# Optimization experiments

Hardware: AMD Instinct MI355X
Metric: run time of the kernel (lower is better)

Reference implementation:

```python
import jax, jax.numpy as jnp
import numpy as np

B, NUMS, SEQ, H, LAYERS, PRED = 128, 128, 256, 1024, 2, 96


def setup_inputs() -> dict:
    key = jax.random.key(0)
    ks = jax.random.split(key, 7)
    s = 0.02
    return {
        "x": jax.random.normal(ks[0], (B, NUMS, SEQ), jnp.float32),
        "W0": jax.random.normal(ks[1], (NUMS + H, 4 * H), jnp.float32) * s,
        "b0": jax.random.normal(ks[2], (4 * H,), jnp.float32) * s,
        "W1": jax.random.normal(ks[3], (H + H, 4 * H), jnp.float32) * s,
        "b1": jax.random.normal(ks[4], (4 * H,), jnp.float32) * s,
        "fc_w": jax.random.normal(ks[5], (H, PRED), jnp.float32) * s,
        "fc_b": jax.random.normal(ks[6], (PRED,), jnp.float32) * s,
    }


def _lstm_layer(x_seq, W, b, h0, c0):
    # x_seq: [B, T, D]; W packs the four gate linears [D+H, 4H] (i,f,o,g)
    def step(carry, xt):
        h, c = carry
        z = jnp.concatenate([xt, h], axis=1) @ W + b  # [B, 4H]
        i, f, o, g = jnp.split(z, 4, axis=1)
        i, f, o = jax.nn.sigmoid(i), jax.nn.sigmoid(f), jax.nn.sigmoid(o)
        c = f * c + i * jnp.tanh(g)
        h = o * jnp.tanh(c)
        return (h, c), h

    (h, c), hs = jax.lax.scan(step, (h0, c0), jnp.swapaxes(x_seq, 0, 1))
    return jnp.swapaxes(hs, 0, 1), h, c  # [B, T, H], [B, H], [B, H]


def reference(x, W0, b0, W1, b1, fc_w, fc_b):
    bsz = x.shape[0]
    h = jnp.zeros((bsz, H), x.dtype)
    c = jnp.zeros((bsz, H), x.dtype)
    seq = jnp.swapaxes(x, 1, 2)  # [B, T, NUMS]
    # NB: faithful to source, (h, c) carry over across layers (no reset)
    seq, h, c = _lstm_layer(seq, W0, b0, h, c)
    seq, h, c = _lstm_layer(seq, W1, b1, h, c)
    out = jnp.tanh(seq[:, -1, :] @ fc_w + fc_b)  # [B, PRED]
    return (out, h, c)
```

## Files before the change

### kernel.cpp

```cpp
#include <hip/hip_runtime.h>
#include <stdint.h>

#define Bsz  128
#define NUMS 128
#define SEQn 256
#define Hn   1024
#define PRED 96
#define G4H  4096
#define GN   256
#define BH   ((size_t)Bsz*Hn)

typedef __attribute__((ext_vector_type(8))) short bf16x8;
typedef __attribute__((ext_vector_type(4))) float f32x4;

template<int N> struct IC { static constexpr int value = N; };

__device__ __forceinline__ unsigned short f2bf(float x){
  union { float f; unsigned u; } v; v.f = x;
  return (unsigned short)((v.u + 0x7FFFu + ((v.u >> 16) & 1u)) >> 16);
}

__global__ void pack_x_kernel(const float* __restrict__ x, unsigned short* __restrict__ xp){
  __shared__ float tile[64][65];
  const int t0 = blockIdx.x * 64, n0 = blockIdx.y * 64, b = blockIdx.z;
  const int tid = threadIdx.x;
  const int c = tid & 63, r = tid >> 6;
  #pragma unroll
  for (int i = 0; i < 16; i++){
    int n = r + i*4;
    tile[n][c] = x[((size_t)b*NUMS + n0 + n)*SEQn + t0 + c];
  }
  __syncthreads();
  #pragma unroll
  for (int i = 0; i < 16; i++){
    int t = r + i*4;
    xp[((size_t)(t0+t)*Bsz + b)*NUMS + n0 + c] = f2bf(tile[c][t]);
  }
}

__global__ void pack_w_kernel(const float* __restrict__ W, unsigned short* __restrict__ Wpk,
                              int KST, int row_off, int kstride, int kof){
  const int u = blockIdx.x * blockDim.x + threadIdx.x;
  if (u >= 256*KST*64) return;
  const int lane = u & 63;
  const int kst  = (u >> 6) % KST;
  const int cgg  = (u >> 6) / KST;
  const int nb = cgg >> 2, gate = cgg & 3;
  const int col = gate*Hn + nb*16 + (lane & 15);
  const int kbase = row_off + kst*32 + (lane >> 4)*8;
  unsigned short tmp[8];
  #pragma unroll
  for (int e = 0; e < 8; e++) tmp[e] = f2bf(W[(size_t)(kbase+e)*G4H + col]);
  ((ulonglong2*)Wpk)[(size_t)(cgg*kstride + kof + kst)*64 + lane] = *(const ulonglong2*)tmp;
}

__global__ void zero_kernel(unsigned short* __restrict__ h0, float* __restrict__ c,
                            unsigned* __restrict__ bars){
  int i = blockIdx.x*256 + threadIdx.x;
  if (i < Bsz*Hn){ h0[i] = 0; c[i] = 0.0f; }
  if (i < 2048) bars[i] = 0u;
}

template<int K1, int S2, int KTOT, int LAYER, bool RING2>
__global__ __launch_bounds__(512, 2)
void persist_kernel(const unsigned short* __restrict__ xpp,
                    unsigned short* __restrict__ hring,
                    unsigned short* __restrict__ h1b,
                    const unsigned short* __restrict__ Wpk,
                    const float* __restrict__ bias,
                    float* __restrict__ cst,
                    float* __restrict__ hf_out,
                    unsigned* __restrict__ bar)
{
  constexpr int KST_TOT = KTOT/32;
  constexpr int HALF = KST_TOT/2;
  constexpr int NCH = (KTOT + 511)/512;
  constexpr int NBUF = (LAYER == 0) ? 2 : 4;
  __shared__ unsigned short sa[NBUF][32*512];
  __shared__ unsigned short sxb[(LAYER == 0) ? 32*128 : 64];
  __shared__ float se[2][4*32*18];

  const int tid = threadIdx.x;
  const int w = tid >> 6, l = tid & 63;
  const int blk = blockIdx.x;
  const int q = blk >> 3;
  const int nb = (blk & 7)*8 + (q & 7);
  const int mb = q >> 3;
  const int ksh = w & 1, cgi = w >> 1;
  const int cgg = nb*4 + cgi;
  const int lrow = l & 15, lg = l >> 4;
  const int bgrp = blk >> 3;

  bf16x8 wreg[HALF];
  #pragma unroll
  for (int j = 0; j < HALF; j++)
    wreg[j] = *(const bf16x8*)(Wpk + ((size_t)(cgg*KST_TOT + 2*j + ksh)*64 + l)*8);

  const int erow = tid >> 4, ejj = tid & 15;
  const int R = mb*32 + erow;
  const int J = nb*16 + ejj;
  const size_t idx = (size_t)R*Hn + J;
  float creg = (LAYER == 0) ? 0.f : cst[idx];

  for (int t = 0; t < SEQn; ++t){
    #pragma unroll
    for (int j = 0; j < HALF; j++) asm volatile("" : "+v"(wreg[j]));

    const unsigned short* A1;
    const unsigned short* A2;
    unsigned short* hout;
    if (LAYER == 0){
      A1   = hring + (size_t)t*BH;
      A2   = xpp + (size_t)t*Bsz*NUMS;
      hout = hring + (size_t)(t+1)*BH;
    } else {
      A1   = hring + (size_t)(t+1)*BH;
      A2   = (t == 0) ? (hring + (size_t)SEQn*BH)
                      : (h1b + (size_t)(RING2 ? (t-1) : ((t-1)&1))*BH);
      hout = h1b + (size_t)(RING2 ? t : (t&1))*BH;
    }

    f32x4 acc2[2] = {{0.f,0.f,0.f,0.f},{0.f,0.f,0.f,0.f}};

    auto stage = [&](int ch, int kw, int lu,
                     const unsigned short* A1p, const unsigned short* A2p){
      unsigned short* dst = (LAYER == 0 && ch == NCH-1) ? sxb : sa[ch];
      const int nissue = kw >> 4;
      for (int i = w; i < nissue; i += 8){
        const int s = i*64 + l;
        const int row = s >> lu;
        const int uu  = s & ((1 << lu) - 1);
        const int ku  = uu ^ (row & 7);
        const int kg  = ch*512 + ku*8;
        const int Rr  = mb*32 + row;
        if (kg < K1){
          const unsigned short* src = A1p + (size_t)Rr*K1 + kg;
          __builtin_amdgcn_global_load_lds(
            (const __attribute__((address_space(1))) void*)src,
            (__attribute__((address_space(3))) void*)&dst[i*512], 16, 0, 0);
        } else {
          const unsigned short* src = A2p + (size_t)Rr*S2 + (kg - K1);
          if constexpr (LAYER == 1 && !RING2){
            __builtin_amdgcn_global_load_lds(
              (const __attribute__((address_space(1))) void*)src,
              (__attribute__((address_space(3))) void*)&dst[i*512], 16, 0, 17);
          } else {
            __builtin_amdgcn_global_load_lds(
              (const __attribute__((address_space(1))) void*)src,
              (__attribute__((address_space(3))) void*)&dst[i*512], 16, 0, 0);
          }
        }
      }
    };

    auto comp = [&](auto CHC){
      constexpr int ch = decltype(CHC)::value;
      if constexpr (ch < NCH){
        constexpr bool isx = (LAYER == 0 && ch == NCH-1);
        constexpr int kw   = isx ? 128 : 512;
        constexpr int UPR  = kw >> 3;
        constexpr int nksl = kw >> 6;
        const unsigned short* abase = isx ? sxb : sa[ch];
        #pragma unroll
        for (int ksl = 0; ksl < nksl; ksl++){
          const int klocal = ksl*2 + ksh;
          const int unit = klocal*4 + lg;
          bf16x8 af0 = *(const bf16x8*)&abase[((lrow     )*UPR + (unit ^ (lrow & 7)))*8];
          bf16x8 af1 = *(const bf16x8*)&abase[((lrow + 16)*UPR + (unit ^ (lrow & 7)))*8];
          acc2[0] = __builtin_amdgcn_mfma_f32_16x16x32_bf16(af0, wreg[ch*8 + ksl], acc2[0], 0, 0, 0);
          acc2[1] = __builtin_amdgcn_mfma_f32_16x16x32_bf16(af1, wreg[ch*8 + ksl], acc2[1], 0, 0, 0);
        }
      }
    };

    if (t == 0){
      stage(0, 512, 6, A1, A2); stage(1, 512, 6, A1, A2);
      if constexpr (LAYER == 1){ stage(2, 512, 6, A1, A2); stage(3, 512, 6, A1, A2); }
      else                       stage(2, 128, 4, A1, A2);
      __syncthreads();
      comp(IC<0>{}); comp(IC<1>{}); comp(IC<2>{}); comp(IC<3>{});
    } else if constexpr (LAYER == 1){
      stage(2, 512, 6, A1, A2); stage(3, 512, 6, A1, A2);
      comp(IC<0>{}); comp(IC<1>{});
      __syncthreads();
      comp(IC<2>{}); comp(IC<3>{});
    } else {
      stage(0, 512, 6, A1, A2); stage(1, 512, 6, A1, A2);
      comp(IC<2>{});
      __syncthreads();
      comp(IC<0>{}); comp(IC<1>{});
    }

    {
      #pragma unroll
      for (int mi = 0; mi < 2; mi++)
        #pragma unroll
        for (int r = 0; r < 4; r++){
          const int row2 = mi*16 + lg*4 + r;
          se[ksh][(cgi*32 + row2)*18 + lrow] = acc2[mi][r];
        }
    }
    __syncthreads();
    {
      float zi = se[0][(0*32+erow)*18 + ejj] + se[1][(0*32+erow)*18 + ejj];
      float zf = se[0][(1*32+erow)*18 + ejj] + se[1][(1*32+erow)*18 + ejj];
      float zo = se[0][(2*32+erow)*18 + ejj] + se[1][(2*32+erow)*18 + ejj];
      float zg = se[0][(3*32+erow)*18 + ejj] + se[1][(3*32+erow)*18 + ejj];
      zi += bias[0*Hn + J]; zf += bias[1*Hn + J];
      zo += bias[2*Hn + J]; zg += bias[3*Hn + J];
      const float gi = 1.f/(1.f + __expf(-zi));
      const float gf = 1.f/(1.f + __expf(-zf));
      const float go = 1.f/(1.f + __expf(-zo));
      const float gg = tanhf(zg);
      creg = gf * creg + gi * gg;
      const float hn = go * tanhf(creg);
      const unsigned hu   = (unsigned)f2bf(hn);
      const unsigned mate = (unsigned)__shfl_xor((int)hu, 1);
      if ((l & 1) == 0){
        const unsigned pk = hu | (mate << 16);
        __hip_atomic_store((unsigned*)(hout + idx), pk,
                           __ATOMIC_RELAXED, __HIP_MEMORY_SCOPE_AGENT);
      }
      if (t == SEQn-1){
        cst[idx] = creg;
        if (LAYER == 1) hf_out[idx] = hn;
      }
    }

    if (t + 1 < SEQn){
      __syncthreads();
      if (tid == 0){
        const unsigned ga = __hip_atomic_fetch_add(&bar[bgrp*16], 1u,
                              __ATOMIC_RELAXED, __HIP_MEMORY_SCOPE_AGENT);
        if (ga == (unsigned)(t*8 + 7)){
          const unsigned ra = __hip_atomic_fetch_add(&bar[512], 1u,
                                __ATOMIC_RELAXED, __HIP_MEMORY_SCOPE_AGENT);
          if (ra == (unsigned)(t*32 + 31))
            __hip_atomic_store(&bar[528], (unsigned)(t+1),
                               __ATOMIC_RELAXED, __HIP_MEMORY_SCOPE_AGENT);
        }
      }
      if constexpr (LAYER == 1){
        const unsigned short* A1n = hring + (size_t)(t+2)*BH;
        stage(0, 512, 6, A1n, A1n);
        stage(1, 512, 6, A1n, A1n);
      } else {
        stage(NCH-1, 128, 4, A1, xpp + (size_t)(t+1)*Bsz*NUMS);
      }
      if (tid == 0){
        while (__hip_atomic_load(&bar[528], __ATOMIC_RELAXED,
                                 __HIP_MEMORY_SCOPE_AGENT) < (unsigned)(t+1))
          __builtin_amdgcn_s_sleep(1);
      }
      __syncthreads();
    }
  }
}

__global__ __launch_bounds__(256)
void fc_out_kernel(const float* __restrict__ hf, const float* __restrict__ cst,
                   const float* __restrict__ fcw, const float* __restrict__ fcb,
                   float* __restrict__ dout){
  __shared__ float hrow[Hn];
  const int b = blockIdx.x, tid = threadIdx.x;
  for (int i = tid; i < Hn; i += 256) hrow[i] = hf[(size_t)b*Hn + i];
  __syncthreads();
  if (tid < PRED){
    float a = fcb[tid];
    for (int k = 0; k < Hn; k++) a += hrow[k] * fcw[(size_t)k*PRED + tid];
    dout[(size_t)b*PRED + tid] = tanhf(a);
  }
  for (int i = tid; i < Hn; i += 256){
    dout[Bsz*PRED + (size_t)b*Hn + i] = hf[(size_t)b*Hn + i];
    dout[Bsz*PRED + (size_t)Bsz*Hn + (size_t)b*Hn + i] = cst[(size_t)b*Hn + i];
  }
}

extern "C" void kernel_launch(void* const* d_in, const int* in_sizes, int n_in,
                              void* d_out, int out_size, void* d_ws, size_t ws_size,
                              hipStream_t stream){
  const float* x   = (const float*)d_in[0];
  const float* W0  = (const float*)d_in[1];
  const float* b0  = (const float*)d_in[2];
  const float* W1  = (const float*)d_in[3];
  const float* b1  = (const float*)d_in[4];
  const float* fcw = (const float*)d_in[5];
  const float* fcb = (const float*)d_in[6];
  float* dout = (float*)d_out;

  char* p = (char*)d_ws;
  auto alloc = [&](size_t bytes)->void*{
    void* r = (void*)p; p += (bytes + 255) & ~(size_t)255; return r;
  };
  unsigned short* xp   = (unsigned short*)alloc((size_t)SEQn*Bsz*NUMS*2);
  unsigned short* Wpk0 = (unsigned short*)alloc((size_t)256*36*64*8*2);
  unsigned short* Wpk1 = (unsigned short*)alloc((size_t)256*64*64*8*2);
  unsigned short* H0   = (unsigned short*)alloc((size_t)(SEQn+1)*BH*2);
  float* cst = (float*)alloc((size_t)BH*4);
  float* hf  = (float*)alloc((size_t)BH*4);
  unsigned* bars = (unsigned*)alloc((size_t)2048*sizeof(unsigned));

  const bool big = ws_size >= (size_t)176*1024*1024;
  unsigned short* h1b;
  if (big) h1b = (unsigned short*)alloc((size_t)SEQn*BH*2);
  else     h1b = (unsigned short*)alloc((size_t)2*BH*2);

  pack_x_kernel<<<dim3(SEQn/64, NUMS/64, Bsz), dim3(256), 0, stream>>>(x, xp);
  pack_w_kernel<<<dim3((256*32*64 + 255)/256), dim3(256), 0, stream>>>(W0, Wpk0, 32, 128, 36, 0);
  pack_w_kernel<<<dim3((256*4*64  + 255)/256), dim3(256), 0, stream>>>(W0, Wpk0,  4,   0, 36, 32);
  pack_w_kernel<<<dim3((256*64*64 + 255)/256), dim3(256), 0, stream>>>(W1, Wpk1, 64, 0, 64, 0);
  zero_kernel<<<dim3((Bsz*Hn + 255)/256), dim3(256), 0, stream>>>(H0, cst, bars);

  persist_kernel<1024, NUMS, 1152, 0, false><<<dim3(GN), dim3(512), 0, stream>>>(
      xp, H0, nullptr, Wpk0, b0, cst, nullptr, bars);

  if (big){
    persist_kernel<1024, Hn, 2048, 1, true><<<dim3(GN), dim3(512), 0, stream>>>(
        nullptr, H0, h1b, Wpk1, b1, cst, hf, bars + 1024);
  } else {
    persist_kernel<1024, Hn, 2048, 1, false><<<dim3(GN), dim3(512), 0, stream>>>(
        nullptr, H0, h1b, Wpk1, b1, cst, hf, bars + 1024);
  }

  fc_out_kernel<<<dim3(Bsz), dim3(256), 0, stream>>>(hf, cst, fcw, fcb, dout);
}
```

Measured before the change: 3.424 ms.

## Stage A tiles in MFMA fragment order with precomputed offsets; use fast tanh

Replaces the generic swizzled staging loop with precomputed per-wave global offsets. Each global_load_lds now writes a contiguous 64-lane fragment that the MFMA reads directly as ((k*2+mi)*64+l), removing the per-step index arithmetic and XOR swizzle math. This cuts per-timestep address computation and branching inside the sequential recurrence loop, which sits on the latency-critical path. It also replaces tanhf with an exp-based fast tanh, which trades some accuracy and saturation behaviour at large inputs for fewer instructions.

```diff
diff --git a/kernel.cpp b/kernel.cpp
--- a/kernel.cpp
+++ b/kernel.cpp
@@ -18,6 +18,9 @@
 __device__ __forceinline__ unsigned short f2bf(float x){
   union { float f; unsigned u; } v; v.f = x;
   return (unsigned short)((v.u + 0x7FFFu + ((v.u >> 16) & 1u)) >> 16);
+}
+__device__ __forceinline__ float fast_tanh(float x){
+  return 1.f - 2.f/(1.f + __expf(2.f*x));
 }
 
 __global__ void pack_x_kernel(const float* __restrict__ x, unsigned short* __restrict__ xp){
@@ -96,11 +99,43 @@
   for (int j = 0; j < HALF; j++)
     wreg[j] = *(const bf16x8*)(Wpk + ((size_t)(cgg*KST_TOT + 2*j + ksh)*64 + l)*8);
 
+  unsigned offA[4];
+  #pragma unroll
+  for (int ii = 0; ii < 4; ii++){
+    const int flat = ii*8 + w;
+    const int kst_l = flat >> 1, mi = flat & 1;
+    offA[ii] = (unsigned)((mb*32 + mi*16 + lrow)*1024 + kst_l*32 + lg*8);
+  }
+  const unsigned offX = (unsigned)((mb*32 + (w & 1)*16 + lrow)*S2 + (w >> 1)*32 + lg*8);
+
   const int erow = tid >> 4, ejj = tid & 15;
   const int R = mb*32 + erow;
   const int J = nb*16 + ejj;
   const size_t idx = (size_t)R*Hn + J;
   float creg = (LAYER == 0) ? 0.f : cst[idx];
+
+  auto stageF = [&](auto CHC, const unsigned short* tilebase){
+    constexpr int ch = decltype(CHC)::value;
+    constexpr bool coh = (LAYER == 1 && !RING2 && ch >= 2);
+    const unsigned short* b2 = tilebase + (ch & 1)*512;
+    #pragma unroll
+    for (int ii = 0; ii < 4; ii++){
+      const unsigned short* src = b2 + offA[ii];
+      if constexpr (coh)
+        __builtin_amdgcn_global_load_lds(
+          (const __attribute__((address_space(1))) void*)src,
+          (__attribute__((address_space(3))) void*)&sa[ch][(ii*8 + w)*512], 16, 0, 17);
+      else
+        __builtin_amdgcn_global_load_lds(
+          (const __attribute__((address_space(1))) void*)src,
+          (__attribute__((address_space(3))) void*)&sa[ch][(ii*8 + w)*512], 16, 0, 0);
+    }
+  };
+  auto stageX = [&](const unsigned short* xbase){
+    __builtin_amdgcn_global_load_lds(
+      (const __attribute__((address_space(1))) void*)(xbase + offX),
+      (__attribute__((address_space(3))) void*)&sxb[w*512], 16, 0, 0);
+  };
 
   for (int t = 0; t < SEQn; ++t){
     #pragma unroll
@@ -122,70 +157,37 @@
 
     f32x4 acc2[2] = {{0.f,0.f,0.f,0.f},{0.f,0.f,0.f,0.f}};
 
-    auto stage = [&](int ch, int kw, int lu,
-                     const unsigned short* A1p, const unsigned short* A2p){
-      unsigned short* dst = (LAYER == 0 && ch == NCH-1) ? sxb : sa[ch];
-      const int nissue = kw >> 4;
-      for (int i = w; i < nissue; i += 8){
-        const int s = i*64 + l;
-        const int row = s >> lu;
-        const int uu  = s & ((1 << lu) - 1);
-        const int ku  = uu ^ (row & 7);
-        const int kg  = ch*512 + ku*8;
-        const int Rr  = mb*32 + row;
-        if (kg < K1){
-          const unsigned short* src = A1p + (size_t)Rr*K1 + kg;
-          __builtin_amdgcn_global_load_lds(
-            (const __attribute__((address_space(1))) void*)src,
-            (__attribute__((address_space(3))) void*)&dst[i*512], 16, 0, 0);
-        } else {
-          const unsigned short* src = A2p + (size_t)Rr*S2 + (kg - K1);
-          if constexpr (LAYER == 1 && !RING2){
-            __builtin_amdgcn_global_load_lds(
-              (const __attribute__((address_space(1))) void*)src,
-              (__attribute__((address_space(3))) void*)&dst[i*512], 16, 0, 17);
-          } else {
-            __builtin_amdgcn_global_load_lds(
-              (const __attribute__((address_space(1))) void*)src,
-              (__attribute__((address_space(3))) void*)&dst[i*512], 16, 0, 0);
-          }
-        }
-      }
-    };
-
     auto comp = [&](auto CHC){
       constexpr int ch = decltype(CHC)::value;
       if constexpr (ch < NCH){
         constexpr bool isx = (LAYER == 0 && ch == NCH-1);
-        constexpr int kw   = isx ? 128 : 512;
-        constexpr int UPR  = kw >> 3;
-        constexpr int nksl = kw >> 6;
-        const unsigned short* abase = isx ? sxb : sa[ch];
+        constexpr int nksl = isx ? 2 : 8;
+        const unsigned short* ab = isx ? sxb : sa[ch];
         #pragma unroll
         for (int ksl = 0; ksl < nksl; ksl++){
           const int klocal = ksl*2 + ksh;
-          const int unit = klocal*4 + lg;
-          bf16x8 af0 = *(const bf16x8*)&abase[((lrow     )*UPR + (unit ^ (lrow & 7)))*8];
-          bf16x8 af1 = *(const bf16x8*)&abase[((lrow + 16)*UPR + (unit ^ (lrow & 7)))*8];
-          acc2[0] = __builtin_amdgcn_mfma_f32_16x16x32_bf16(af0, wreg[ch*8 + ksl], acc2[0], 0, 0, 0);
-          acc2[1] = __builtin_amdgcn_mfma_f32_16x16x32_bf16(af1, wreg[ch*8 + ksl], acc2[1], 0, 0, 0);
+          const int wj = isx ? (16 + ksl) : (ch*8 + ksl);
+          bf16x8 af0 = *(const bf16x8*)&ab[((klocal*2 + 0)*64 + l)*8];
+          bf16x8 af1 = *(const bf16x8*)&ab[((klocal*2 + 1)*64 + l)*8];
+          acc2[0] = __builtin_amdgcn_mfma_f32_16x16x32_bf16(af0, wreg[wj], acc2[0], 0, 0, 0);
+          acc2[1] = __builtin_amdgcn_mfma_f32_16x16x32_bf16(af1, wreg[wj], acc2[1], 0, 0, 0);
         }
       }
     };
 
     if (t == 0){
-      stage(0, 512, 6, A1, A2); stage(1, 512, 6, A1, A2);
-      if constexpr (LAYER == 1){ stage(2, 512, 6, A1, A2); stage(3, 512, 6, A1, A2); }
-      else                       stage(2, 128, 4, A1, A2);
+      stageF(IC<0>{}, A1); stageF(IC<1>{}, A1);
+      if constexpr (LAYER == 1){ stageF(IC<2>{}, A2); stageF(IC<3>{}, A2); }
+      else                       stageX(A2);
       __syncthreads();
       comp(IC<0>{}); comp(IC<1>{}); comp(IC<2>{}); comp(IC<3>{});
     } else if constexpr (LAYER == 1){
-      stage(2, 512, 6, A1, A2); stage(3, 512, 6, A1, A2);
+      stageF(IC<2>{}, A2); stageF(IC<3>{}, A2);
       comp(IC<0>{}); comp(IC<1>{});
       __syncthreads();
       comp(IC<2>{}); comp(IC<3>{});
     } else {
-      stage(0, 512, 6, A1, A2); stage(1, 512, 6, A1, A2);
+      stageF(IC<0>{}, A1); stageF(IC<1>{}, A1);
       comp(IC<2>{});
       __syncthreads();
       comp(IC<0>{}); comp(IC<1>{});
@@ -211,9 +213,9 @@
       const float gi = 1.f/(1.f + __expf(-zi));
       const float gf = 1.f/(1.f + __expf(-zf));
       const float go = 1.f/(1.f + __expf(-zo));
-      const float gg = tanhf(zg);
+      const float gg = fast_tanh(zg);
       creg = gf * creg + gi * gg;
-      const float hn = go * tanhf(creg);
+      const float hn = go * fast_tanh(creg);
       const unsigned hu   = (unsigned)f2bf(hn);
       const unsigned mate = (unsigned)__shfl_xor((int)hu, 1);
       if ((l & 1) == 0){
@@ -242,10 +244,10 @@
       }
       if constexpr (LAYER == 1){
         const unsigned short* A1n = hring + (size_t)(t+2)*BH;
-        stage(0, 512, 6, A1n, A1n);
-        stage(1, 512, 6, A1n, A1n);
+        stageF(IC<0>{}, A1n);
+        stageF(IC<1>{}, A1n);
       } else {
-        stage(NCH-1, 128, 4, A1, xpp + (size_t)(t+1)*Bsz*NUMS);
+        stageX(xpp + (size_t)(t+1)*Bsz*NUMS);
       }
       if (tid == 0){
         while (__hip_atomic_load(&bar[528], __ATOMIC_RELAXED,
```

After: 3.373 ms. About the same (-1.5%).
